# Kernel tuning notes

Hardware: AMD Instinct MI355X
Metric: run time of the kernel (lower is better)

## Reference

```python
import jax, jax.numpy as jnp
import numpy as np

D_MODEL = 1024
N_HEADS = 16
HEAD_DIM = D_MODEL // N_HEADS


def setup_inputs() -> dict:
    key = jax.random.key(0)
    k1, k2, k3 = jax.random.split(key, 3)
    x = jax.random.normal(k1, (4, 2048, D_MODEL), dtype=jnp.float32)
    # torch Linear(d, 3d, bias=False): y = x @ W.T ; store transposed weight [d, 3d]
    scale = 1.0 / np.sqrt(D_MODEL)
    W_qkv = jax.random.normal(k2, (D_MODEL, 3 * D_MODEL), dtype=jnp.float32) * scale
    W_proj = jax.random.normal(k3, (D_MODEL, D_MODEL), dtype=jnp.float32) * scale
    return {"x": x, "W_qkv": W_qkv, "W_proj": W_proj}


def reference(x, W_qkv, W_proj):
    B, T, C = x.shape
    h, d = N_HEADS, HEAD_DIM
    qkv = x @ W_qkv                      # [B,T,3C]
    q, k, v = jnp.split(qkv, 3, axis=-1)
    def split_heads(t):
        return t.reshape(B, T, h, d).transpose(0, 2, 1, 3)  # [B,h,T,d]
    q, k, v = map(split_heads, (q, k, v))
    att = jnp.einsum('bhqd,bhkd->bhqk', q, k) / np.sqrt(d)  # [B,h,T,T]
    causal = jnp.tril(jnp.ones((T, T), dtype=bool))
    att = jnp.where(causal, att, -jnp.inf)
    att = jax.nn.softmax(att, axis=-1)
    # dropout = 0.0 (eval mode): no-op
    y = jnp.einsum('bhqk,bhkd->bhqd', att, v)               # [B,h,T,d]
    y = y.transpose(0, 2, 1, 3).reshape(B, T, C)
    return y @ W_proj
```

## Files before the change

kernel.cpp:

```cpp
#include <hip/hip_runtime.h>

#define T_SEQ 2048
#define D_MODEL 1024
#define NB 4
#define NH 16
#define HD 64

typedef __attribute__((ext_vector_type(8))) __bf16 bf16x8;
typedef __attribute__((ext_vector_type(4))) __bf16 bf16x4;
typedef __attribute__((ext_vector_type(4))) float f32x4;

__device__ __forceinline__ void gload_lds16(const void* g, void* l) {
  __builtin_amdgcn_global_load_lds((const __attribute__((address_space(1))) unsigned int*)g,
                                   (__attribute__((address_space(3))) unsigned int*)l,
                                   16, 0, 0);
}

__device__ __forceinline__ unsigned int pack_bf16_2(float e0, float e1) {
  unsigned short u0 = __builtin_bit_cast(unsigned short, (__bf16)e0);
  unsigned short u1 = __builtin_bit_cast(unsigned short, (__bf16)e1);
  return (unsigned int)u0 | ((unsigned int)u1 << 16);
}

__global__ __launch_bounds__(256) void cvt_bf16_kernel(const float* __restrict__ s,
                                                       __bf16* __restrict__ d, int n) {
  int i = (blockIdx.x * 256 + threadIdx.x) * 8;
  if (i >= n) return;
  float4 a = *(const float4*)(s + i);
  float4 b = *(const float4*)(s + i + 4);
  bf16x8 v;
  v[0] = (__bf16)a.x; v[1] = (__bf16)a.y; v[2] = (__bf16)a.z; v[3] = (__bf16)a.w;
  v[4] = (__bf16)b.x; v[5] = (__bf16)b.y; v[6] = (__bf16)b.z; v[7] = (__bf16)b.w;
  *(bf16x8*)(d + i) = v;
}

__global__ __launch_bounds__(256) void transpose_cvt_kernel(const float* __restrict__ W,
                                                            __bf16* __restrict__ Wt,
                                                            int K, int N) {
  __shared__ float t[32][33];
  int tx = threadIdx.x, ty = threadIdx.y;
  int n0 = blockIdx.x * 32, k0 = blockIdx.y * 32;
#pragma unroll
  for (int r = 0; r < 4; ++r)
    t[ty + r * 8][tx] = W[(size_t)(k0 + ty + r * 8) * N + n0 + tx];
  __syncthreads();
#pragma unroll
  for (int r = 0; r < 4; ++r)
    Wt[(size_t)(n0 + ty + r * 8) * K + k0 + tx] = (__bf16)t[tx][ty + r * 8];
}

__global__ __launch_bounds__(256) void extract_vt_kernel(const __bf16* __restrict__ qkv,
                                                         __bf16* __restrict__ Vt) {
  __shared__ __bf16 t[32][34];
  int tx = threadIdx.x, ty = threadIdx.y;
  int tt = blockIdx.x * 32;
  int dt = blockIdx.y * 32;
  int bh = blockIdx.z;
  int b = bh >> 4, h = bh & 15;
#pragma unroll
  for (int r = 0; r < 4; ++r)
    t[ty + r * 8][tx] = qkv[(size_t)(b * T_SEQ + tt + ty + r * 8) * 3072 + 2048 + h * HD + dt + tx];
  __syncthreads();
#pragma unroll
  for (int r = 0; r < 4; ++r)
    Vt[(size_t)(bh * HD + dt + ty + r * 8) * T_SEQ + tt + tx] = t[tx][ty + r * 8];
}

template <typename OutT>
__global__ __launch_bounds__(256) void gemm_bt(const __bf16* __restrict__ A,
                                               const __bf16* __restrict__ Bt,
                                               OutT* __restrict__ C,
                                               int M, int N, int K) {
  __shared__ __bf16 lA[128 * 64];
  __shared__ __bf16 lB[128 * 64];
  int tid = threadIdx.x;
  int lane = tid & 63, w = tid >> 6;
  int wm = w >> 1, wn = w & 1;
  int nwgx = gridDim.x;
  int lid = blockIdx.y * nwgx + blockIdx.x;
  int cpx = (nwgx * gridDim.y) >> 3;
  int swz = (lid & 7) * cpx + (lid >> 3);
  int bn = swz % nwgx, bm = swz / nwgx;
  f32x4 acc[4][4] = {};
  for (int kt = 0; kt < K; kt += 64) {
#pragma unroll
    for (int it = 0; it < 4; ++it) {
      int o = it * 4096 + tid * 16;
      int row = o >> 7;
      int ss = ((o >> 4) & 7) ^ (row & 7);
      gload_lds16(A + (size_t)(bm * 128 + row) * K + kt + ss * 8, (char*)lA + o);
      gload_lds16(Bt + (size_t)(bn * 128 + row) * K + kt + ss * 8, (char*)lB + o);
    }
    __syncthreads();
    bf16x8 af[4][2], bfv[4][2];
#pragma unroll
    for (int i = 0; i < 4; ++i)
#pragma unroll
      for (int kk = 0; kk < 2; ++kk) {
        int ra = wm * 64 + i * 16 + (lane & 15);
        int sa = ((lane >> 4) + kk * 4) ^ (ra & 7);
        af[i][kk] = *(const bf16x8*)((const char*)lA + ra * 128 + sa * 16);
        int rb = wn * 64 + i * 16 + (lane & 15);
        int sb = ((lane >> 4) + kk * 4) ^ (rb & 7);
        bfv[i][kk] = *(const bf16x8*)((const char*)lB + rb * 128 + sb * 16);
      }
#pragma unroll
    for (int kk = 0; kk < 2; ++kk)
#pragma unroll
      for (int i = 0; i < 4; ++i)
#pragma unroll
        for (int j = 0; j < 4; ++j)
          acc[i][j] = __builtin_amdgcn_mfma_f32_16x16x32_bf16(af[i][kk], bfv[j][kk], acc[i][j], 0, 0, 0);
    __syncthreads();
  }
#pragma unroll
  for (int i = 0; i < 4; ++i)
#pragma unroll
    for (int j = 0; j < 4; ++j)
#pragma unroll
      for (int r = 0; r < 4; ++r) {
        int row = bm * 128 + wm * 64 + i * 16 + (lane >> 4) * 4 + r;
        int col = bn * 128 + wn * 64 + j * 16 + (lane & 15);
        C[(size_t)row * N + col] = (OutT)acc[i][j][r];
      }
}

__global__ __launch_bounds__(256, 4) void attn_kernel(const __bf16* __restrict__ qkv,
                                                      const __bf16* __restrict__ Vt,
                                                      __bf16* __restrict__ Y) {
  __shared__ __bf16 lK[2][64 * 64];
  __shared__ __bf16 lV[2][64 * 64];
  int tid = threadIdx.x, lane = tid & 63, w = tid >> 6;
  int q = lane & 15, g = lane >> 4;
  int wl = w & 1;

  int l = blockIdx.x;
  int pairHB = ((l & 7) << 3) | (l >> 7);
  int p = (l >> 3) & 15;
  int h = pairHB & 15, b = pairHB >> 4;
  int qtHi = 31 - p;
  int myqt = (w < 2) ? qtHi : p;

  const float SCALE = 0.125f * 1.44269504088896f;
  const f32x4 fzero = {0.f, 0.f, 0.f, 0.f};

  bf16x8 qf[2][2];
#pragma unroll
  for (int qi = 0; qi < 2; ++qi) {
    const __bf16* qp =
        qkv + (size_t)(b * T_SEQ + myqt * 64 + wl * 32 + qi * 16 + q) * 3072 + h * HD;
    qf[qi][0] = *(const bf16x8*)(qp + g * 8);
    qf[qi][1] = *(const bf16x8*)(qp + 32 + g * 8);
#pragma unroll
    for (int kk = 0; kk < 2; ++kk)
#pragma unroll
      for (int jj = 0; jj < 8; ++jj)
        qf[qi][kk][jj] = (__bf16)((float)qf[qi][kk][jj] * SCALE);
  }

  float m[2] = {-INFINITY, -INFINITY}, lsum[2] = {0.f, 0.f};
  f32x4 yacc[2][4];
#pragma unroll
  for (int qi = 0; qi < 2; ++qi)
#pragma unroll
    for (int f = 0; f < 4; ++f) yacc[qi][f] = fzero;

  asm volatile("s_waitcnt vmcnt(0)" ::: "memory");
  __builtin_amdgcn_sched_barrier(0);

  auto STAGE = [&](int kvt, int bi) {
#pragma unroll
    for (int it = 0; it < 2; ++it) {
      int o = it * 4096 + tid * 16;
      int row = o >> 7;
      int ss = ((o >> 4) & 7) ^ (row & 7);
      gload_lds16(qkv + (size_t)(b * T_SEQ + kvt * 64 + row) * 3072 + 1024 + h * HD + ss * 8,
                  (char*)lK[bi] + o);
      gload_lds16(Vt + (size_t)((b * NH + h) * HD + row) * T_SEQ + kvt * 64 + ss * 8,
                  (char*)lV[bi] + o);
    }
  };

  STAGE(0, 0);

#pragma unroll 1
  for (int kvt = 0; kvt <= qtHi; ++kvt) {
    int cur = kvt & 1;
    if (kvt < qtHi) {
      STAGE(kvt + 1, cur ^ 1);
      asm volatile("s_waitcnt vmcnt(4)" ::: "memory");
    } else {
      asm volatile("s_waitcnt vmcnt(0)" ::: "memory");
    }
    __builtin_amdgcn_sched_barrier(0);
    __builtin_amdgcn_s_barrier();
    __builtin_amdgcn_sched_barrier(0);

    if (kvt <= myqt) {
      f32x4 s[2][4];
#pragma unroll
      for (int qi = 0; qi < 2; ++qi)
#pragma unroll
        for (int f = 0; f < 4; ++f) s[qi][f] = fzero;
      const char* Kbase = (const char*)lK[cur];
      __builtin_amdgcn_s_setprio(1);
#pragma unroll
      for (int kk = 0; kk < 2; ++kk)
#pragma unroll
        for (int f = 0; f < 4; ++f) {
          int rk = f * 16 + q;
          int sk = (g + kk * 4) ^ (rk & 7);
          bf16x8 kf = *(const bf16x8*)(Kbase + rk * 128 + sk * 16);
#pragma unroll
          for (int qi = 0; qi < 2; ++qi)
            s[qi][f] = __builtin_amdgcn_mfma_f32_16x16x32_bf16(kf, qf[qi][kk], s[qi][f], 0, 0, 0);
        }
      __builtin_amdgcn_s_setprio(0);

      if (kvt == myqt) {
#pragma unroll
        for (int qi = 0; qi < 2; ++qi) {
          int qloc = wl * 32 + qi * 16 + q;
#pragma unroll
          for (int f = 0; f < 4; ++f)
#pragma unroll
            for (int r = 0; r < 4; ++r)
              if (f * 16 + g * 4 + r > qloc) s[qi][f][r] = -INFINITY;
        }
      }

      float mx[2];
#pragma unroll
      for (int qi = 0; qi < 2; ++qi) {
        float v = fmaxf(fmaxf(fmaxf(s[qi][0][0], s[qi][0][1]), fmaxf(s[qi][0][2], s[qi][0][3])),
                        fmaxf(fmaxf(s[qi][1][0], s[qi][1][1]), fmaxf(s[qi][1][2], s[qi][1][3])));
        v = fmaxf(v, fmaxf(fmaxf(fmaxf(s[qi][2][0], s[qi][2][1]), fmaxf(s[qi][2][2], s[qi][2][3])),
                           fmaxf(fmaxf(s[qi][3][0], s[qi][3][1]), fmaxf(s[qi][3][2], s[qi][3][3]))));
        v = fmaxf(v, __shfl_xor(v, 16, 64));
        v = fmaxf(v, __shfl_xor(v, 32, 64));
        mx[qi] = v;
      }

      float growth = fmaxf(mx[0] - m[0], mx[1] - m[1]);
      if (__any(growth > 8.0f)) {
#pragma unroll
        for (int qi = 0; qi < 2; ++qi) {
          float mn = fmaxf(m[qi], mx[qi]);
          float al = exp2f(m[qi] - mn);
          m[qi] = mn;
          lsum[qi] *= al;
#pragma unroll
          for (int r = 0; r < 4; ++r) {
            float ar = __shfl(al, g * 4 + r, 64);
#pragma unroll
            for (int f = 0; f < 4; ++f) yacc[qi][f][r] *= ar;
          }
        }
      }

      unsigned int Wd[2][4][2];
#pragma unroll
      for (int qi = 0; qi < 2; ++qi) {
        float ps = 0.f;
#pragma unroll
        for (int f = 0; f < 4; ++f)
#pragma unroll
          for (int hh = 0; hh < 2; ++hh) {
            float e0 = exp2f(s[qi][f][2 * hh] - m[qi]);
            float e1 = exp2f(s[qi][f][2 * hh + 1] - m[qi]);
            ps += e0 + e1;
            Wd[qi][f][hh] = pack_bf16_2(e0, e1);
          }
        lsum[qi] += ps;
      }

      int srcA = ((g & 1) << 5) | q;
      int srcB = srcA + 16;
      bool hisel = (g >= 2);
      bf16x8 pa[2][2];
#pragma unroll
      for (int qi = 0; qi < 2; ++qi)
#pragma unroll
        for (int kk = 0; kk < 2; ++kk) {
          unsigned int pw[4];
#pragma unroll
          for (int t = 0; t < 4; ++t) {
            int src = (t < 2) ? srcA : srcB;
            unsigned int c0 = (unsigned int)__shfl((int)Wd[qi][2 * kk][t & 1], src, 64);
            unsigned int c1 = (unsigned int)__shfl((int)Wd[qi][2 * kk + 1][t & 1], src, 64);
            pw[t] = hisel ? c1 : c0;
          }
          uint4 u = make_uint4(pw[0], pw[1], pw[2], pw[3]);
          pa[qi][kk] = __builtin_bit_cast(bf16x8, u);
        }

      const char* Vbase = (const char*)lV[cur];
      __builtin_amdgcn_s_setprio(1);
#pragma unroll
      for (int kk = 0; kk < 2; ++kk)
#pragma unroll
        for (int f = 0; f < 4; ++f) {
          int rv = f * 16 + q;
          int sv2 = (g + kk * 4) ^ (rv & 7);
          bf16x8 vf = *(const bf16x8*)(Vbase + rv * 128 + sv2 * 16);
#pragma unroll
          for (int qi = 0; qi < 2; ++qi)
            yacc[qi][f] = __builtin_amdgcn_mfma_f32_16x16x32_bf16(pa[qi][kk], vf, yacc[qi][f], 0, 0, 0);
        }
      __builtin_amdgcn_s_setprio(0);
    }

    __builtin_amdgcn_sched_barrier(0);
    asm volatile("s_waitcnt lgkmcnt(0)" ::: "memory");
    __builtin_amdgcn_s_barrier();
    __builtin_amdgcn_sched_barrier(0);
  }

#pragma unroll
  for (int qi = 0; qi < 2; ++qi) {
    float ls = lsum[qi];
    ls += __shfl_xor(ls, 16, 64);
    ls += __shfl_xor(ls, 32, 64);
    float linv = 1.0f / ls;
    int qrow = myqt * 64 + wl * 32 + qi * 16 + g * 4;
#pragma unroll
    for (int r = 0; r < 4; ++r) {
      float lr = __shfl(linv, g * 4 + r, 64);
#pragma unroll
      for (int f = 0; f < 4; ++f) {
        Y[(size_t)(b * T_SEQ + qrow + r) * D_MODEL + h * HD + f * 16 + q] =
            (__bf16)(yacc[qi][f][r] * lr);
      }
    }
  }
}

extern "C" void kernel_launch(void* const* d_in, const int* in_sizes, int n_in,
                              void* d_out, int out_size, void* d_ws, size_t ws_size,
                              hipStream_t stream) {
  const float* x = (const float*)d_in[0];
  const float* Wqkv = (const float*)d_in[1];
  const float* Wproj = (const float*)d_in[2];
  float* out = (float*)d_out;
  char* ws = (char*)d_ws;

  __bf16* Xbf     = (__bf16*)(ws);
  __bf16* Wqkv_t  = (__bf16*)(ws + 16777216);
  __bf16* Wproj_t = (__bf16*)(ws + 23068672);
  __bf16* QKV     = (__bf16*)(ws + 25165824);
  __bf16* Vt      = (__bf16*)(ws + 75497472);
  __bf16* Yb      = (__bf16*)(ws + 92274688);

  cvt_bf16_kernel<<<4096, 256, 0, stream>>>(x, Xbf, NB * T_SEQ * D_MODEL);
  transpose_cvt_kernel<<<dim3(96, 32), dim3(32, 8), 0, stream>>>(Wqkv, Wqkv_t, 1024, 3072);
  transpose_cvt_kernel<<<dim3(32, 32), dim3(32, 8), 0, stream>>>(Wproj, Wproj_t, 1024, 1024);
  gemm_bt<__bf16><<<dim3(24, 64), 256, 0, stream>>>(Xbf, Wqkv_t, QKV, 8192, 3072, 1024);
  extract_vt_kernel<<<dim3(64, 2, 64), dim3(32, 8), 0, stream>>>(QKV, Vt);
  attn_kernel<<<1024, 256, 0, stream>>>(QKV, Vt, Yb);
  gemm_bt<float><<<dim3(8, 64), 256, 0, stream>>>(Yb, Wproj_t, out, 8192, 1024, 1024);
}
```

Before: 305.7 us.

## Balance causal attention work by giving each wave rows from both query tiles

Previously waves 0-1 handled the high query tile and waves 2-3 the low tile, so the low-tile waves sat idle for most KV iterations. Now every wave owns 16 rows of the high tile and 16 rows of the low tile. Each wave runs a two-tile step while the KV index is within the low tile, and a single-tile step afterwards, which spreads MFMA work evenly across waves. K and V LDS buffers are merged into one array with precomputed swizzled addresses, and the softmax rescale check now runs per tile instead of jointly.

```diff
diff --git a/kernel.cpp b/kernel.cpp
--- a/kernel.cpp
+++ b/kernel.cpp
@@ -125,21 +125,129 @@
       }
 }
 
+template <int NQ>
+__device__ __forceinline__ void attn_step(
+    const char* base, int a0, int a1,
+    const bf16x8 (&qf)[2][2], f32x4 (&yacc)[2][4], float (&m)[2], float (&lsum)[2],
+    int q, int g, int w, bool diag0, bool diag1, int srcA, int srcB, bool hisel) {
+  const f32x4 fzero = {0.f, 0.f, 0.f, 0.f};
+  f32x4 s[NQ][4];
+#pragma unroll
+  for (int qi = 0; qi < NQ; ++qi)
+#pragma unroll
+    for (int f = 0; f < 4; ++f) s[qi][f] = fzero;
+  __builtin_amdgcn_s_setprio(1);
+#pragma unroll
+  for (int kk = 0; kk < 2; ++kk) {
+    int aa = kk ? a1 : a0;
+#pragma unroll
+    for (int f = 0; f < 4; ++f) {
+      bf16x8 kf = *(const bf16x8*)(base + aa + f * 2048);
+#pragma unroll
+      for (int qi = 0; qi < NQ; ++qi)
+        s[qi][f] = __builtin_amdgcn_mfma_f32_16x16x32_bf16(kf, qf[qi][kk], s[qi][f], 0, 0, 0);
+    }
+  }
+  __builtin_amdgcn_s_setprio(0);
+
+  int qloc = w * 16 + q;
+  if (diag0) {
+#pragma unroll
+    for (int f = 0; f < 4; ++f)
+#pragma unroll
+      for (int r = 0; r < 4; ++r)
+        if (f * 16 + g * 4 + r > qloc) s[0][f][r] = -INFINITY;
+  }
+  if (NQ == 2 && diag1) {
+#pragma unroll
+    for (int f = 0; f < 4; ++f)
+#pragma unroll
+      for (int r = 0; r < 4; ++r)
+        if (f * 16 + g * 4 + r > qloc) s[1][f][r] = -INFINITY;
+  }
+
+  unsigned int Wd[NQ][4][2];
+#pragma unroll
+  for (int qi = 0; qi < NQ; ++qi) {
+    float mx = fmaxf(fmaxf(s[qi][0][0], s[qi][0][1]), s[qi][0][2]);
+    mx = fmaxf(fmaxf(mx, s[qi][0][3]), s[qi][1][0]);
+    mx = fmaxf(fmaxf(mx, s[qi][1][1]), s[qi][1][2]);
+    mx = fmaxf(fmaxf(mx, s[qi][1][3]), s[qi][2][0]);
+    mx = fmaxf(fmaxf(mx, s[qi][2][1]), s[qi][2][2]);
+    mx = fmaxf(fmaxf(mx, s[qi][2][3]), s[qi][3][0]);
+    mx = fmaxf(fmaxf(mx, s[qi][3][1]), s[qi][3][2]);
+    mx = fmaxf(mx, s[qi][3][3]);
+    mx = fmaxf(mx, __shfl_xor(mx, 16, 64));
+    mx = fmaxf(mx, __shfl_xor(mx, 32, 64));
+    if (__any(mx - m[qi] > 8.0f)) {
+      float mn = fmaxf(m[qi], mx);
+      float al = exp2f(m[qi] - mn);
+      m[qi] = mn;
+      lsum[qi] *= al;
+#pragma unroll
+      for (int r = 0; r < 4; ++r) {
+        float ar = __shfl(al, g * 4 + r, 64);
+#pragma unroll
+        for (int f = 0; f < 4; ++f) yacc[qi][f][r] *= ar;
+      }
+    }
+    float ps = 0.f;
+#pragma unroll
+    for (int f = 0; f < 4; ++f)
+#pragma unroll
+      for (int hh = 0; hh < 2; ++hh) {
+        float e0 = exp2f(s[qi][f][2 * hh] - m[qi]);
+        float e1 = exp2f(s[qi][f][2 * hh + 1] - m[qi]);
+        ps += e0 + e1;
+        Wd[qi][f][hh] = pack_bf16_2(e0, e1);
+      }
+    lsum[qi] += ps;
+  }
+
+  bf16x8 pa[NQ][2];
+#pragma unroll
+  for (int qi = 0; qi < NQ; ++qi)
+#pragma unroll
+    for (int kk = 0; kk < 2; ++kk) {
+      unsigned int pw[4];
+#pragma unroll
+      for (int t = 0; t < 4; ++t) {
+        int src = (t < 2) ? srcA : srcB;
+        unsigned int c0 = (unsigned int)__shfl((int)Wd[qi][2 * kk][t & 1], src, 64);
+        unsigned int c1 = (unsigned int)__shfl((int)Wd[qi][2 * kk + 1][t & 1], src, 64);
+        pw[t] = hisel ? c1 : c0;
+      }
+      uint4 u = make_uint4(pw[0], pw[1], pw[2], pw[3]);
+      pa[qi][kk] = __builtin_bit_cast(bf16x8, u);
+    }
+
+  __builtin_amdgcn_s_setprio(1);
+#pragma unroll
+  for (int kk = 0; kk < 2; ++kk) {
+    int aa = kk ? a1 : a0;
+#pragma unroll
+    for (int f = 0; f < 4; ++f) {
+      bf16x8 vf = *(const bf16x8*)(base + 8192 + aa + f * 2048);
+#pragma unroll
+      for (int qi = 0; qi < NQ; ++qi)
+        yacc[qi][f] = __builtin_amdgcn_mfma_f32_16x16x32_bf16(pa[qi][kk], vf, yacc[qi][f], 0, 0, 0);
+    }
+  }
+  __builtin_amdgcn_s_setprio(0);
+}
+
 __global__ __launch_bounds__(256, 4) void attn_kernel(const __bf16* __restrict__ qkv,
                                                       const __bf16* __restrict__ Vt,
                                                       __bf16* __restrict__ Y) {
-  __shared__ __bf16 lK[2][64 * 64];
-  __shared__ __bf16 lV[2][64 * 64];
+  __shared__ __bf16 lKV[2][2][64 * 64];
   int tid = threadIdx.x, lane = tid & 63, w = tid >> 6;
   int q = lane & 15, g = lane >> 4;
-  int wl = w & 1;
 
   int l = blockIdx.x;
   int pairHB = ((l & 7) << 3) | (l >> 7);
   int p = (l >> 3) & 15;
   int h = pairHB & 15, b = pairHB >> 4;
-  int qtHi = 31 - p;
-  int myqt = (w < 2) ? qtHi : p;
+  int qtHi = 31 - p, qtLo = p;
 
   const float SCALE = 0.125f * 1.44269504088896f;
   const f32x4 fzero = {0.f, 0.f, 0.f, 0.f};
@@ -147,8 +255,8 @@
   bf16x8 qf[2][2];
 #pragma unroll
   for (int qi = 0; qi < 2; ++qi) {
-    const __bf16* qp =
-        qkv + (size_t)(b * T_SEQ + myqt * 64 + wl * 32 + qi * 16 + q) * 3072 + h * HD;
+    int qt = qi ? qtLo : qtHi;
+    const __bf16* qp = qkv + (size_t)(b * T_SEQ + qt * 64 + w * 16 + q) * 3072 + h * HD;
     qf[qi][0] = *(const bf16x8*)(qp + g * 8);
     qf[qi][1] = *(const bf16x8*)(qp + 32 + g * 8);
 #pragma unroll
@@ -164,6 +272,12 @@
   for (int qi = 0; qi < 2; ++qi)
 #pragma unroll
     for (int f = 0; f < 4; ++f) yacc[qi][f] = fzero;
+
+  int a0 = q * 128 + ((g ^ (q & 7)) << 4);
+  int a1 = a0 ^ 64;
+  int srcA = ((g & 1) << 5) | q;
+  int srcB = srcA + 16;
+  bool hisel = (g >= 2);
 
   asm volatile("s_waitcnt vmcnt(0)" ::: "memory");
   __builtin_amdgcn_sched_barrier(0);
@@ -175,9 +289,9 @@
       int row = o >> 7;
       int ss = ((o >> 4) & 7) ^ (row & 7);
       gload_lds16(qkv + (size_t)(b * T_SEQ + kvt * 64 + row) * 3072 + 1024 + h * HD + ss * 8,
-                  (char*)lK[bi] + o);
+                  (char*)&lKV[bi][0][0] + o);
       gload_lds16(Vt + (size_t)((b * NH + h) * HD + row) * T_SEQ + kvt * 64 + ss * 8,
-                  (char*)lV[bi] + o);
+                  (char*)&lKV[bi][1][0] + o);
     }
   };
 
@@ -196,118 +310,13 @@
     __builtin_amdgcn_s_barrier();
     __builtin_amdgcn_sched_barrier(0);
 
-    if (kvt <= myqt) {
-      f32x4 s[2][4];
-#pragma unroll
-      for (int qi = 0; qi < 2; ++qi)
-#pragma unroll
-        for (int f = 0; f < 4; ++f) s[qi][f] = fzero;
-      const char* Kbase = (const char*)lK[cur];
-      __builtin_amdgcn_s_setprio(1);
-#pragma unroll
-      for (int kk = 0; kk < 2; ++kk)
-#pragma unroll
-        for (int f = 0; f < 4; ++f) {
-          int rk = f * 16 + q;
-          int sk = (g + kk * 4) ^ (rk & 7);
-          bf16x8 kf = *(const bf16x8*)(Kbase + rk * 128 + sk * 16);
-#pragma unroll
-          for (int qi = 0; qi < 2; ++qi)
-            s[qi][f] = __builtin_amdgcn_mfma_f32_16x16x32_bf16(kf, qf[qi][kk], s[qi][f], 0, 0, 0);
-        }
-      __builtin_amdgcn_s_setprio(0);
-
-      if (kvt == myqt) {
-#pragma unroll
-        for (int qi = 0; qi < 2; ++qi) {
-          int qloc = wl * 32 + qi * 16 + q;
-#pragma unroll
-          for (int f = 0; f < 4; ++f)
-#pragma unroll
-            for (int r = 0; r < 4; ++r)
-              if (f * 16 + g * 4 + r > qloc) s[qi][f][r] = -INFINITY;
-        }
-      }
-
-      float mx[2];
-#pragma unroll
-      for (int qi = 0; qi < 2; ++qi) {
-        float v = fmaxf(fmaxf(fmaxf(s[qi][0][0], s[qi][0][1]), fmaxf(s[qi][0][2], s[qi][0][3])),
-                        fmaxf(fmaxf(s[qi][1][0], s[qi][1][1]), fmaxf(s[qi][1][2], s[qi][1][3])));
-        v = fmaxf(v, fmaxf(fmaxf(fmaxf(s[qi][2][0], s[qi][2][1]), fmaxf(s[qi][2][2], s[qi][2][3])),
-                           fmaxf(fmaxf(s[qi][3][0], s[qi][3][1]), fmaxf(s[qi][3][2], s[qi][3][3]))));
-        v = fmaxf(v, __shfl_xor(v, 16, 64));
-        v = fmaxf(v, __shfl_xor(v, 32, 64));
-        mx[qi] = v;
-      }
-
-      float growth = fmaxf(mx[0] - m[0], mx[1] - m[1]);
-      if (__any(growth > 8.0f)) {
-#pragma unroll
-        for (int qi = 0; qi < 2; ++qi) {
-          float mn = fmaxf(m[qi], mx[qi]);
-          float al = exp2f(m[qi] - mn);
-          m[qi] = mn;
-          lsum[qi] *= al;
-#pragma unroll
-          for (int r = 0; r < 4; ++r) {
-            float ar = __shfl(al, g * 4 + r, 64);
-#pragma unroll
-            for (int f = 0; f < 4; ++f) yacc[qi][f][r] *= ar;
-          }
-        }
-      }
-
-      unsigned int Wd[2][4][2];
-#pragma unroll
-      for (int qi = 0; qi < 2; ++qi) {
-        float ps = 0.f;
-#pragma unroll
-        for (int f = 0; f < 4; ++f)
-#pragma unroll
-          for (int hh = 0; hh < 2; ++hh) {
-            float e0 = exp2f(s[qi][f][2 * hh] - m[qi]);
-            float e1 = exp2f(s[qi][f][2 * hh + 1] - m[qi]);
-            ps += e0 + e1;
-            Wd[qi][f][hh] = pack_bf16_2(e0, e1);
-          }
-        lsum[qi] += ps;
-      }
-
-      int srcA = ((g & 1) << 5) | q;
-      int srcB = srcA + 16;
-      bool hisel = (g >= 2);
-      bf16x8 pa[2][2];
-#pragma unroll
-      for (int qi = 0; qi < 2; ++qi)
-#pragma unroll
-        for (int kk = 0; kk < 2; ++kk) {
-          unsigned int pw[4];
-#pragma unroll
-          for (int t = 0; t < 4; ++t) {
-            int src = (t < 2) ? srcA : srcB;
-            unsigned int c0 = (unsigned int)__shfl((int)Wd[qi][2 * kk][t & 1], src, 64);
-            unsigned int c1 = (unsigned int)__shfl((int)Wd[qi][2 * kk + 1][t & 1], src, 64);
-            pw[t] = hisel ? c1 : c0;
-          }
-          uint4 u = make_uint4(pw[0], pw[1], pw[2], pw[3]);
-          pa[qi][kk] = __builtin_bit_cast(bf16x8, u);
-        }
-
-      const char* Vbase = (const char*)lV[cur];
-      __builtin_amdgcn_s_setprio(1);
-#pragma unroll
-      for (int kk = 0; kk < 2; ++kk)
-#pragma unroll
-        for (int f = 0; f < 4; ++f) {
-          int rv = f * 16 + q;
-          int sv2 = (g + kk * 4) ^ (rv & 7);
-          bf16x8 vf = *(const bf16x8*)(Vbase + rv * 128 + sv2 * 16);
-#pragma unroll
-          for (int qi = 0; qi < 2; ++qi)
-            yacc[qi][f] = __builtin_amdgcn_mfma_f32_16x16x32_bf16(pa[qi][kk], vf, yacc[qi][f], 0, 0, 0);
-        }
-      __builtin_amdgcn_s_setprio(0);
+    const char* base = (const char*)lKV + cur * 16384;
+    if (kvt <= qtLo) {
+      attn_step<2>(base, a0, a1, qf, yacc, m, lsum, q, g, w,
+                   false, (kvt == qtLo), srcA, srcB, hisel);
+    } else {
+      attn_step<1>(base, a0, a1, qf, yacc, m, lsum, q, g, w,
+                   (kvt == qtHi), false, srcA, srcB, hisel);
     }
 
     __builtin_amdgcn_sched_barrier(0);
@@ -318,11 +327,12 @@
 
 #pragma unroll
   for (int qi = 0; qi < 2; ++qi) {
+    int qt = qi ? qtLo : qtHi;
     float ls = lsum[qi];
     ls += __shfl_xor(ls, 16, 64);
     ls += __shfl_xor(ls, 32, 64);
     float linv = 1.0f / ls;
-    int qrow = myqt * 64 + wl * 32 + qi * 16 + g * 4;
+    int qrow = qt * 64 + w * 16 + g * 4;
 #pragma unroll
     for (int r = 0; r < 4; ++r) {
       float lr = __shfl(linv, g * 4 + r, 64);
```

Measured after the change: 303.5 us. About the same (-0.7%).
